# Kernel optimization log

Hardware: AMD Instinct MI355X
Metric: run time of the kernel (lower is better)

Reference implementation:

```python
import jax, jax.numpy as jnp
import numpy as np

FP8_MAX = 448.0  # torch.finfo(float8_e4m3fn).max
BLK = 128
EPS = 1e-12

def fp8_round(x):
    # saturated cast to float8_e4m3fn and back (emulates to_fp8_saturated)
    y = jnp.clip(x, -FP8_MAX, FP8_MAX)
    return y.astype(jnp.float8_e4m3fn).astype(jnp.float32)

def per_tile_quant_dequant(x):
    # activation: 1x128 tiles along the feature dim
    S, D = x.shape
    t = x.reshape(S, D // BLK, BLK)
    amax = jnp.max(jnp.abs(t), axis=-1, keepdims=True)
    scale = jnp.maximum(amax, EPS) / FP8_MAX
    q = fp8_round(t / scale)
    return (q * scale).reshape(S, D)

def per_block_quant_dequant_weight(w):
    # weight: 128x128 blocks, w is [ne, dout, din]
    ne, do, di = w.shape
    blk = w.reshape(ne, do // BLK, BLK, di // BLK, BLK)
    amax = jnp.max(jnp.abs(blk), axis=(2, 4), keepdims=True)
    scale = jnp.maximum(amax, EPS) / FP8_MAX
    q = fp8_round(blk / scale)
    return (q * scale).reshape(ne, do, di)

def setup_inputs() -> dict:
    key = jax.random.key(0)
    k1, k2 = jax.random.split(key)
    NE, DOUT, DIN, SEQ = 8, 1024, 2048, 16384
    x = jax.random.normal(k1, (SEQ, DIN), dtype=jnp.float32)
    w = jax.random.normal(k2, (NE * DOUT, DIN), dtype=jnp.float32) * 0.02
    tokens_per_expert = jnp.full((NE,), SEQ // NE, dtype=jnp.int32)
    return {"input": x, "tokens_per_expert": tokens_per_expert, "weight": w}

def reference(input, tokens_per_expert, weight):
    NE = tokens_per_expert.shape[0]
    S, DIN = input.shape
    DOUT = weight.shape[0] // NE
    w = weight.reshape(NE, DOUT, DIN)
    w_dq = per_block_quant_dequant_weight(w)   # fp8 per-block weight, dequantized
    x_dq = per_tile_quant_dequant(input)       # fp8 per-tile activation, dequantized
    # grouped varlen GEMM; tokens are split equally across experts here
    T = S // NE
    xe = x_dq.reshape(NE, T, DIN)
    out = jnp.einsum('etd,eod->eto', xe, w_dq)  # [ne, T, dout]
    return out.reshape(S, DOUT)
```

## Files before the change

kernel.cpp:

```cpp
#include <hip/hip_runtime.h>
#include <hip/hip_bf16.h>
#include <hip/hip_fp8.h>

#define SEQ   16384
#define DIN_  2048
#define DOUT_ 1024
#define NE_   8
#define TPE   (SEQ / NE_)
#define NG    (DIN_ / 128)

typedef float f32x4 __attribute__((ext_vector_type(4)));
typedef int   i32x4 __attribute__((ext_vector_type(4)));
typedef int   i32x8 __attribute__((ext_vector_type(8)));

#define GLD(gp, lp) __builtin_amdgcn_global_load_lds( \
    (const __attribute__((address_space(1))) unsigned int*)(gp), \
    (__attribute__((address_space(3))) unsigned int*)(lp), 16, 0, 0)

__device__ __forceinline__ unsigned char fp8_byte(float v, float scale) {
    float r = v / scale;
    r = fminf(fmaxf(r, -448.0f), 448.0f);
    __hip_fp8_e4m3 q(r);
    return (unsigned char)q.__x;
}

__global__ __launch_bounds__(256) void quant_x_kernel(const float* __restrict__ X,
                                                      unsigned char* __restrict__ Xq,
                                                      float* __restrict__ sxT) {
    const int row  = blockIdx.x;
    const int t    = threadIdx.x;
    const int lane = t & 63;
    const int wave = t >> 6;
    const int tile = wave * 4 + (lane >> 4);
    const int sub  = lane & 15;

    const float* p = X + (size_t)row * DIN_ + tile * 128 + sub * 8;
    float4 v0 = *(const float4*)p;
    float4 v1 = *(const float4*)(p + 4);

    float m = fmaxf(fmaxf(fmaxf(fabsf(v0.x), fabsf(v0.y)), fmaxf(fabsf(v0.z), fabsf(v0.w))),
                    fmaxf(fmaxf(fabsf(v1.x), fabsf(v1.y)), fmaxf(fabsf(v1.z), fabsf(v1.w))));
    #pragma unroll
    for (int off = 1; off < 16; off <<= 1)
        m = fmaxf(m, __shfl_xor(m, off, 64));

    const float scale = fmaxf(m, 1e-12f) / 448.0f;
    if (sub == 0) sxT[(size_t)tile * SEQ + row] = scale;

    unsigned lo = (unsigned)fp8_byte(v0.x, scale)
                | ((unsigned)fp8_byte(v0.y, scale) << 8)
                | ((unsigned)fp8_byte(v0.z, scale) << 16)
                | ((unsigned)fp8_byte(v0.w, scale) << 24);
    unsigned hi = (unsigned)fp8_byte(v1.x, scale)
                | ((unsigned)fp8_byte(v1.y, scale) << 8)
                | ((unsigned)fp8_byte(v1.z, scale) << 16)
                | ((unsigned)fp8_byte(v1.w, scale) << 24);
    uint2 u; u.x = lo; u.y = hi;
    *(uint2*)(Xq + (size_t)row * DIN_ + tile * 128 + sub * 8) = u;
}

__global__ __launch_bounds__(256) void quant_w_kernel(const float* __restrict__ W,
                                                      unsigned char* __restrict__ Wq,
                                                      float* __restrict__ sw) {
    const int rb = blockIdx.x >> 4;
    const int cb = blockIdx.x & 15;
    const int t  = threadIdx.x;

    const float* base = W + (size_t)(rb * 128) * DIN_ + cb * 128;
    const int r0 = t >> 5;
    const int c0 = (t & 31) * 4;

    float4 v[16];
    float m = 0.0f;
    #pragma unroll
    for (int i = 0; i < 16; ++i) {
        v[i] = *(const float4*)(base + (size_t)(i * 8 + r0) * DIN_ + c0);
        m = fmaxf(m, fmaxf(fmaxf(fabsf(v[i].x), fabsf(v[i].y)),
                           fmaxf(fabsf(v[i].z), fabsf(v[i].w))));
    }
    #pragma unroll
    for (int off = 1; off < 64; off <<= 1)
        m = fmaxf(m, __shfl_xor(m, off, 64));
    __shared__ float smx[4];
    if ((t & 63) == 0) smx[t >> 6] = m;
    __syncthreads();
    const float amax  = fmaxf(fmaxf(smx[0], smx[1]), fmaxf(smx[2], smx[3]));
    const float scale = fmaxf(amax, 1e-12f) / 448.0f;
    if (t == 0) sw[rb * 16 + cb] = scale;

    unsigned char* obase = Wq + (size_t)(rb * 128) * DIN_ + cb * 128;
    #pragma unroll
    for (int i = 0; i < 16; ++i) {
        unsigned u = (unsigned)fp8_byte(v[i].x, scale)
                   | ((unsigned)fp8_byte(v[i].y, scale) << 8)
                   | ((unsigned)fp8_byte(v[i].z, scale) << 16)
                   | ((unsigned)fp8_byte(v[i].w, scale) << 24);
        *(unsigned int*)(obase + (size_t)(i * 8 + r0) * DIN_ + c0) = u;
    }
}

__global__ __launch_bounds__(512, 2) void gemm_kernel(const unsigned char* __restrict__ Xq,
                                                      const unsigned char* __restrict__ Wq,
                                                      const float* __restrict__ sxT,
                                                      const float* __restrict__ sw,
                                                      float* __restrict__ out) {
    __shared__ unsigned char lds[147456];

    const int bid  = blockIdx.x;
    const int wgid = (bid & 7) * 32 + (bid >> 3);
    const int e    = wgid >> 5;
    const int tile = wgid & 31;
    const int brow = tile >> 2;
    const int bcol = tile & 3;

    const int t    = threadIdx.x;
    const int lane = t & 63;
    const int wave = t >> 6;
    const int wm   = wave >> 2;
    const int wn   = wave & 3;

    const int row0 = e * TPE + brow * 256;
    const unsigned char* Xt = Xq + (size_t)row0 * DIN_;
    const unsigned char* Wt = Wq + (size_t)(e * DOUT_ + bcol * 256) * DIN_;
    const float* swp = sw + (size_t)(e * 8 + bcol * 2 + (wn >> 1)) * 16;

    auto stage_group = [&](int g) {
        if (g >= NG) return;
        const unsigned abase = (unsigned)(g & 1) * 32768u;
        #pragma unroll
        for (int i = 0; i < 4; ++i) {
            const unsigned p = (unsigned)i * 8192u + (unsigned)t * 16u;
            const unsigned q = p ^ (((p >> 7) & 7u) << 4);
            GLD(Xt + (size_t)(q >> 7) * DIN_ + g * 128 + (q & 127u), &lds[abase + p]);
        }
        #pragma unroll
        for (int i = 0; i < 4; ++i) {
            const unsigned p = (unsigned)i * 8192u + (unsigned)t * 16u;
            const unsigned q = p ^ (((p >> 7) & 7u) << 4);
            GLD(Wt + (size_t)(q >> 7) * DIN_ + g * 128 + (q & 127u), &lds[65536u + abase + p]);
        }
    };

    auto ld_frag = [&](unsigned base, unsigned r) -> i32x8 {
        const unsigned kc  = (unsigned)(lane >> 4);
        const unsigned msk = (r & 7u) << 4;
        const unsigned p0  = (r * 128u + kc * 32u) ^ msk;
        const unsigned p1  = (r * 128u + kc * 32u + 16u) ^ msk;
        i32x4 lo = *(const i32x4*)&lds[base + p0];
        i32x4 hi = *(const i32x4*)&lds[base + p1];
        return __builtin_shufflevector(lo, hi, 0, 1, 2, 3, 4, 5, 6, 7);
    };
    auto ld_sx = [&](int m, int g) -> f32x4 {
        const unsigned r = (unsigned)(wm * 128 + m * 16 + ((lane >> 4) << 2));
        return *(const f32x4*)&lds[131072u + (unsigned)g * 1024u + r * 4u];
    };

    f32x4 acc[8][4] = {};
    const f32x4 zero = {0.f, 0.f, 0.f, 0.f};

    #pragma unroll
    for (int i = 0; i < 2; ++i) {
        const unsigned p = (unsigned)i * 8192u + (unsigned)t * 16u;
        GLD((const unsigned char*)sxT + ((size_t)(p >> 10) * SEQ + row0) * 4 + (p & 1023u),
            &lds[131072u + p]);
    }
    stage_group(0);
    stage_group(1);
    asm volatile("s_waitcnt vmcnt(8)" ::: "memory");
    __builtin_amdgcn_s_barrier();

    for (int g = 0; g < NG; ++g) {
        const unsigned abase = (unsigned)(g & 1) * 32768u;
        const unsigned bbase = 65536u + abase;
        const float swg = __uint_as_float(
            __builtin_amdgcn_readfirstlane(__float_as_uint(swp[g])));

        i32x8 bfr[4];
        #pragma unroll
        for (int n = 0; n < 4; ++n)
            bfr[n] = ld_frag(bbase, (unsigned)(wn * 64 + n * 16 + (lane & 15)));

        {
            i32x8 afr[4]; f32x4 sxv[4];
            #pragma unroll
            for (int m = 0; m < 4; ++m) {
                afr[m] = ld_frag(abase, (unsigned)(wm * 128 + m * 16 + (lane & 15)));
                sxv[m] = ld_sx(m, g);
            }
            asm volatile("s_waitcnt lgkmcnt(0)" ::: "memory");
            __builtin_amdgcn_sched_barrier(0);
            __builtin_amdgcn_s_setprio(1);
            #pragma unroll
            for (int m = 0; m < 4; ++m) {
                const f32x4 sf = sxv[m] * swg;
                #pragma unroll
                for (int n = 0; n < 4; ++n) {
                    f32x4 pn = __builtin_amdgcn_mfma_scale_f32_16x16x128_f8f6f4(
                        afr[m], bfr[n], zero, 0, 0, 0, 0x7f7f7f7f, 0, 0x7f7f7f7f);
                    acc[m][n] += pn * sf;
                }
            }
            __builtin_amdgcn_s_setprio(0);
        }

        {
            i32x8 afr[4]; f32x4 sxv[4];
            #pragma unroll
            for (int m = 0; m < 4; ++m) {
                afr[m] = ld_frag(abase, (unsigned)(wm * 128 + (m + 4) * 16 + (lane & 15)));
                sxv[m] = ld_sx(m + 4, g);
            }
            asm volatile("s_waitcnt lgkmcnt(0)" ::: "memory");
            __builtin_amdgcn_sched_barrier(0);
            __builtin_amdgcn_s_barrier();
            stage_group(g + 2);
            __builtin_amdgcn_s_setprio(1);
            #pragma unroll
            for (int m = 0; m < 4; ++m) {
                const f32x4 sf = sxv[m] * swg;
                #pragma unroll
                for (int n = 0; n < 4; ++n) {
                    f32x4 pn = __builtin_amdgcn_mfma_scale_f32_16x16x128_f8f6f4(
                        afr[m], bfr[n], zero, 0, 0, 0, 0x7f7f7f7f, 0, 0x7f7f7f7f);
                    acc[m + 4][n] += pn * sf;
                }
            }
            __builtin_amdgcn_s_setprio(0);
        }

        if (g < NG - 1) {
            if (g <= NG - 3)
                asm volatile("s_waitcnt vmcnt(8)" ::: "memory");
            else
                asm volatile("s_waitcnt vmcnt(0)" ::: "memory");
            __builtin_amdgcn_s_barrier();
        }
    }

    const int orow0 = e * TPE + brow * 256 + wm * 128;
    const int ocol0 = bcol * 256 + wn * 64;
    const int rl = (lane >> 4) * 4;
    const int cl = lane & 15;
    #pragma unroll
    for (int m = 0; m < 8; ++m)
        #pragma unroll
        for (int n = 0; n < 4; ++n)
            #pragma unroll
            for (int j = 0; j < 4; ++j) {
                const int r = orow0 + m * 16 + rl + j;
                const int c = ocol0 + n * 16 + cl;
                out[(size_t)r * DOUT_ + c] = acc[m][n][j];
            }
}

extern "C" void kernel_launch(void* const* d_in, const int* in_sizes, int n_in,
                              void* d_out, int out_size, void* d_ws, size_t ws_size,
                              hipStream_t stream) {
    const float* x = (const float*)d_in[0];
    const float* w = (const float*)d_in[2];
    float* out = (float*)d_out;

    unsigned char* xq = (unsigned char*)d_ws;
    unsigned char* wq = xq + (size_t)SEQ * DIN_;
    float* sxT = (float*)(wq + (size_t)NE_ * DOUT_ * DIN_);
    float* sw  = sxT + (size_t)NG * SEQ;

    quant_x_kernel<<<SEQ, 256, 0, stream>>>(x, xq, sxT);
    quant_w_kernel<<<(NE_ * DOUT_ / 128) * (DIN_ / 128), 256, 0, stream>>>(w, wq, sw);
    gemm_kernel<<<NE_ * (TPE / 256) * (DOUT_ / 256), 512, 0, stream>>>(xq, wq, sxT, sw, out);
}
```

Baseline: 140.8 us.

## Restructure GEMM loop schedule, stage weight scales in LDS, batch quant_x rows

The GEMM main loop is reordered. Next-group fragment reads for B, the first half of A and the scales are issued right after the barrier that follows staging. MFMAs are interleaved in pairs, so each scaled accumulate overlaps the next MFMA. Per-block weight scales are preloaded once into LDS instead of read from global each iteration. Separately, quant_x processes 4 rows per block, and both quant kernels multiply by a reciprocal instead of dividing. The reciprocal can change fp8 rounding slightly at boundary values.

```diff
diff --git a/kernel.cpp b/kernel.cpp
--- a/kernel.cpp
+++ b/kernel.cpp
@@ -17,8 +17,8 @@
     (const __attribute__((address_space(1))) unsigned int*)(gp), \
     (__attribute__((address_space(3))) unsigned int*)(lp), 16, 0, 0)
 
-__device__ __forceinline__ unsigned char fp8_byte(float v, float scale) {
-    float r = v / scale;
+__device__ __forceinline__ unsigned char fp8_byte_m(float v, float sinv) {
+    float r = v * sinv;
     r = fminf(fmaxf(r, -448.0f), 448.0f);
     __hip_fp8_e4m3 q(r);
     return (unsigned char)q.__x;
@@ -27,36 +27,48 @@
 __global__ __launch_bounds__(256) void quant_x_kernel(const float* __restrict__ X,
                                                       unsigned char* __restrict__ Xq,
                                                       float* __restrict__ sxT) {
-    const int row  = blockIdx.x;
     const int t    = threadIdx.x;
     const int lane = t & 63;
     const int wave = t >> 6;
     const int tile = wave * 4 + (lane >> 4);
     const int sub  = lane & 15;
-
-    const float* p = X + (size_t)row * DIN_ + tile * 128 + sub * 8;
-    float4 v0 = *(const float4*)p;
-    float4 v1 = *(const float4*)(p + 4);
-
-    float m = fmaxf(fmaxf(fmaxf(fabsf(v0.x), fabsf(v0.y)), fmaxf(fabsf(v0.z), fabsf(v0.w))),
-                    fmaxf(fmaxf(fabsf(v1.x), fabsf(v1.y)), fmaxf(fabsf(v1.z), fabsf(v1.w))));
-    #pragma unroll
-    for (int off = 1; off < 16; off <<= 1)
-        m = fmaxf(m, __shfl_xor(m, off, 64));
-
-    const float scale = fmaxf(m, 1e-12f) / 448.0f;
-    if (sub == 0) sxT[(size_t)tile * SEQ + row] = scale;
-
-    unsigned lo = (unsigned)fp8_byte(v0.x, scale)
-                | ((unsigned)fp8_byte(v0.y, scale) << 8)
-                | ((unsigned)fp8_byte(v0.z, scale) << 16)
-                | ((unsigned)fp8_byte(v0.w, scale) << 24);
-    unsigned hi = (unsigned)fp8_byte(v1.x, scale)
-                | ((unsigned)fp8_byte(v1.y, scale) << 8)
-                | ((unsigned)fp8_byte(v1.z, scale) << 16)
-                | ((unsigned)fp8_byte(v1.w, scale) << 24);
-    uint2 u; u.x = lo; u.y = hi;
-    *(uint2*)(Xq + (size_t)row * DIN_ + tile * 128 + sub * 8) = u;
+    const size_t off = (size_t)tile * 128 + sub * 8;
+
+    const int row0 = blockIdx.x * 4;
+    float4 v0[4], v1[4];
+    float mx[4];
+    #pragma unroll
+    for (int r = 0; r < 4; ++r) {
+        const float* p = X + (size_t)(row0 + r) * DIN_ + off;
+        v0[r] = *(const float4*)p;
+        v1[r] = *(const float4*)(p + 4);
+        mx[r] = fmaxf(fmaxf(fmaxf(fabsf(v0[r].x), fabsf(v0[r].y)),
+                            fmaxf(fabsf(v0[r].z), fabsf(v0[r].w))),
+                      fmaxf(fmaxf(fabsf(v1[r].x), fabsf(v1[r].y)),
+                            fmaxf(fabsf(v1[r].z), fabsf(v1[r].w))));
+    }
+    #pragma unroll
+    for (int o = 1; o < 16; o <<= 1) {
+        #pragma unroll
+        for (int r = 0; r < 4; ++r)
+            mx[r] = fmaxf(mx[r], __shfl_xor(mx[r], o, 64));
+    }
+    #pragma unroll
+    for (int r = 0; r < 4; ++r) {
+        const float s    = fmaxf(mx[r], 1e-12f) / 448.0f;
+        const float sinv = 1.0f / s;
+        if (sub == 0) sxT[(size_t)tile * SEQ + row0 + r] = s;
+        unsigned lo = (unsigned)fp8_byte_m(v0[r].x, sinv)
+                    | ((unsigned)fp8_byte_m(v0[r].y, sinv) << 8)
+                    | ((unsigned)fp8_byte_m(v0[r].z, sinv) << 16)
+                    | ((unsigned)fp8_byte_m(v0[r].w, sinv) << 24);
+        unsigned hi = (unsigned)fp8_byte_m(v1[r].x, sinv)
+                    | ((unsigned)fp8_byte_m(v1[r].y, sinv) << 8)
+                    | ((unsigned)fp8_byte_m(v1[r].z, sinv) << 16)
+                    | ((unsigned)fp8_byte_m(v1[r].w, sinv) << 24);
+        uint2 u; u.x = lo; u.y = hi;
+        *(uint2*)(Xq + (size_t)(row0 + r) * DIN_ + off) = u;
+    }
 }
 
 __global__ __launch_bounds__(256) void quant_w_kernel(const float* __restrict__ W,
@@ -84,17 +96,18 @@
     __shared__ float smx[4];
     if ((t & 63) == 0) smx[t >> 6] = m;
     __syncthreads();
-    const float amax  = fmaxf(fmaxf(smx[0], smx[1]), fmaxf(smx[2], smx[3]));
-    const float scale = fmaxf(amax, 1e-12f) / 448.0f;
-    if (t == 0) sw[rb * 16 + cb] = scale;
+    const float amax = fmaxf(fmaxf(smx[0], smx[1]), fmaxf(smx[2], smx[3]));
+    const float s    = fmaxf(amax, 1e-12f) / 448.0f;
+    const float sinv = 1.0f / s;
+    if (t == 0) sw[rb * 16 + cb] = s;
 
     unsigned char* obase = Wq + (size_t)(rb * 128) * DIN_ + cb * 128;
     #pragma unroll
     for (int i = 0; i < 16; ++i) {
-        unsigned u = (unsigned)fp8_byte(v[i].x, scale)
-                   | ((unsigned)fp8_byte(v[i].y, scale) << 8)
-                   | ((unsigned)fp8_byte(v[i].z, scale) << 16)
-                   | ((unsigned)fp8_byte(v[i].w, scale) << 24);
+        unsigned u = (unsigned)fp8_byte_m(v[i].x, sinv)
+                   | ((unsigned)fp8_byte_m(v[i].y, sinv) << 8)
+                   | ((unsigned)fp8_byte_m(v[i].z, sinv) << 16)
+                   | ((unsigned)fp8_byte_m(v[i].w, sinv) << 24);
         *(unsigned int*)(obase + (size_t)(i * 8 + r0) * DIN_ + c0) = u;
     }
 }
@@ -102,9 +115,9 @@
 __global__ __launch_bounds__(512, 2) void gemm_kernel(const unsigned char* __restrict__ Xq,
                                                       const unsigned char* __restrict__ Wq,
                                                       const float* __restrict__ sxT,
-                                                      const float* __restrict__ sw,
+                                                      const float* __restrict__ swg_,
                                                       float* __restrict__ out) {
-    __shared__ unsigned char lds[147456];
+    __shared__ __align__(16) unsigned char lds[147584];
 
     const int bid  = blockIdx.x;
     const int wgid = (bid & 7) * 32 + (bid >> 3);
@@ -118,45 +131,71 @@
     const int wave = t >> 6;
     const int wm   = wave >> 2;
     const int wn   = wave & 3;
+    const int fl   = lane & 15;
+    const unsigned kc  = (unsigned)(lane >> 4);
+    const unsigned sxr = (unsigned)((lane >> 4) * 4);
 
     const int row0 = e * TPE + brow * 256;
     const unsigned char* Xt = Xq + (size_t)row0 * DIN_;
     const unsigned char* Wt = Wq + (size_t)(e * DOUT_ + bcol * 256) * DIN_;
-    const float* swp = sw + (size_t)(e * 8 + bcol * 2 + (wn >> 1)) * 16;
-
-    auto stage_group = [&](int g) {
-        if (g >= NG) return;
-        const unsigned abase = (unsigned)(g & 1) * 32768u;
+
+    auto stage = [&](int j) {
+        if (j >= NG) return;
+        const unsigned ab = (unsigned)(j & 1) * 32768u;
         #pragma unroll
         for (int i = 0; i < 4; ++i) {
             const unsigned p = (unsigned)i * 8192u + (unsigned)t * 16u;
             const unsigned q = p ^ (((p >> 7) & 7u) << 4);
-            GLD(Xt + (size_t)(q >> 7) * DIN_ + g * 128 + (q & 127u), &lds[abase + p]);
+            GLD(Xt + (size_t)(q >> 7) * DIN_ + j * 128 + (q & 127u), &lds[ab + p]);
         }
         #pragma unroll
         for (int i = 0; i < 4; ++i) {
             const unsigned p = (unsigned)i * 8192u + (unsigned)t * 16u;
             const unsigned q = p ^ (((p >> 7) & 7u) << 4);
-            GLD(Wt + (size_t)(q >> 7) * DIN_ + g * 128 + (q & 127u), &lds[65536u + abase + p]);
+            GLD(Wt + (size_t)(q >> 7) * DIN_ + j * 128 + (q & 127u),
+                &lds[65536u + ab + p]);
         }
     };
 
-    auto ld_frag = [&](unsigned base, unsigned r) -> i32x8 {
-        const unsigned kc  = (unsigned)(lane >> 4);
-        const unsigned msk = (r & 7u) << 4;
-        const unsigned p0  = (r * 128u + kc * 32u) ^ msk;
-        const unsigned p1  = (r * 128u + kc * 32u + 16u) ^ msk;
-        i32x4 lo = *(const i32x4*)&lds[base + p0];
-        i32x4 hi = *(const i32x4*)&lds[base + p1];
+    auto ldf8 = [&](unsigned base, unsigned row) -> i32x8 {
+        const unsigned p0 = row * 128u + kc * 32u;
+        const unsigned s  = ((p0 >> 7) & 7u) << 4;
+        i32x4 lo = *(const i32x4*)&lds[base + (p0 ^ s)];
+        i32x4 hi = *(const i32x4*)&lds[base + ((p0 + 16u) ^ s)];
         return __builtin_shufflevector(lo, hi, 0, 1, 2, 3, 4, 5, 6, 7);
     };
-    auto ld_sx = [&](int m, int g) -> f32x4 {
-        const unsigned r = (unsigned)(wm * 128 + m * 16 + ((lane >> 4) << 2));
-        return *(const f32x4*)&lds[131072u + (unsigned)g * 1024u + r * 4u];
-    };
-
+
+    i32x8 bfr[4], aA[4], aB[4];
+    f32x4 sxv03[4], sxv47[4];
+    float swg;
     f32x4 acc[8][4] = {};
     const f32x4 zero = {0.f, 0.f, 0.f, 0.f};
+
+    #define AB_(buf) ((unsigned)(buf) * 32768u)
+    #define BB_(buf) (65536u + (unsigned)(buf) * 32768u)
+    #define MFS(a, b) __builtin_amdgcn_mfma_scale_f32_16x16x128_f8f6f4( \
+        a, b, zero, 0, 0, 0, 0x7f7f7f7f, 0, 0x7f7f7f7f)
+    #define TOP_READS(buf, g) \
+      { _Pragma("unroll") for (int n_ = 0; n_ < 4; ++n_) \
+            bfr[n_] = ldf8(BB_(buf), (unsigned)(wn * 64 + n_ * 16 + fl)); \
+        _Pragma("unroll") for (int m_ = 0; m_ < 4; ++m_) \
+            aA[m_] = ldf8(AB_(buf), (unsigned)(wm * 128 + m_ * 16 + fl)); \
+        _Pragma("unroll") for (int m_ = 0; m_ < 4; ++m_) \
+            sxv03[m_] = *(const f32x4*)&lds[131072u + (unsigned)(g) * 1024u \
+                + (unsigned)(wm * 128 + m_ * 16) * 4u + sxr * 4u]; \
+        swg = *(const float*)&lds[147456u + (unsigned)(((wn >> 1) << 4) + (g)) * 4u]; }
+    #define PHASE_MFMA(mo, afr, sxv) \
+      { f32x4 pnA[4], pnB[4]; \
+        const f32x4 sf0 = sxv[0] * swg, sf1 = sxv[1] * swg; \
+        const f32x4 sf2 = sxv[2] * swg, sf3 = sxv[3] * swg; \
+        _Pragma("unroll") for (int n_ = 0; n_ < 4; ++n_) pnA[n_] = MFS(afr[0], bfr[n_]); \
+        _Pragma("unroll") for (int n_ = 0; n_ < 4; ++n_) pnB[n_] = MFS(afr[1], bfr[n_]); \
+        _Pragma("unroll") for (int n_ = 0; n_ < 4; ++n_) acc[(mo)+0][n_] += pnA[n_] * sf0; \
+        _Pragma("unroll") for (int n_ = 0; n_ < 4; ++n_) pnA[n_] = MFS(afr[2], bfr[n_]); \
+        _Pragma("unroll") for (int n_ = 0; n_ < 4; ++n_) acc[(mo)+1][n_] += pnB[n_] * sf1; \
+        _Pragma("unroll") for (int n_ = 0; n_ < 4; ++n_) pnB[n_] = MFS(afr[3], bfr[n_]); \
+        _Pragma("unroll") for (int n_ = 0; n_ < 4; ++n_) acc[(mo)+2][n_] += pnA[n_] * sf2; \
+        _Pragma("unroll") for (int n_ = 0; n_ < 4; ++n_) acc[(mo)+3][n_] += pnB[n_] * sf3; }
 
     #pragma unroll
     for (int i = 0; i < 2; ++i) {
@@ -164,76 +203,44 @@
         GLD((const unsigned char*)sxT + ((size_t)(p >> 10) * SEQ + row0) * 4 + (p & 1023u),
             &lds[131072u + p]);
     }
-    stage_group(0);
-    stage_group(1);
+    float swv = 0.0f;
+    if (t < 32) swv = swg_[(size_t)(e * 8 + bcol * 2 + (t >> 4)) * 16 + (t & 15)];
+    stage(0); stage(1);
     asm volatile("s_waitcnt vmcnt(8)" ::: "memory");
+    if (t < 32) *(float*)&lds[147456u + (unsigned)t * 4u] = swv;
+    asm volatile("s_waitcnt lgkmcnt(0)" ::: "memory");
     __builtin_amdgcn_s_barrier();
+    TOP_READS(0, 0)
 
     for (int g = 0; g < NG; ++g) {
-        const unsigned abase = (unsigned)(g & 1) * 32768u;
-        const unsigned bbase = 65536u + abase;
-        const float swg = __uint_as_float(
-            __builtin_amdgcn_readfirstlane(__float_as_uint(swp[g])));
-
-        i32x8 bfr[4];
-        #pragma unroll
-        for (int n = 0; n < 4; ++n)
-            bfr[n] = ld_frag(bbase, (unsigned)(wn * 64 + n * 16 + (lane & 15)));
-
-        {
-            i32x8 afr[4]; f32x4 sxv[4];
-            #pragma unroll
-            for (int m = 0; m < 4; ++m) {
-                afr[m] = ld_frag(abase, (unsigned)(wm * 128 + m * 16 + (lane & 15)));
-                sxv[m] = ld_sx(m, g);
-            }
-            asm volatile("s_waitcnt lgkmcnt(0)" ::: "memory");
-            __builtin_amdgcn_sched_barrier(0);
-            __builtin_amdgcn_s_setprio(1);
-            #pragma unroll
-            for (int m = 0; m < 4; ++m) {
-                const f32x4 sf = sxv[m] * swg;
-                #pragma unroll
-                for (int n = 0; n < 4; ++n) {
-                    f32x4 pn = __builtin_amdgcn_mfma_scale_f32_16x16x128_f8f6f4(
-                        afr[m], bfr[n], zero, 0, 0, 0, 0x7f7f7f7f, 0, 0x7f7f7f7f);
-                    acc[m][n] += pn * sf;
-                }
-            }
-            __builtin_amdgcn_s_setprio(0);
-        }
-
-        {
-            i32x8 afr[4]; f32x4 sxv[4];
-            #pragma unroll
-            for (int m = 0; m < 4; ++m) {
-                afr[m] = ld_frag(abase, (unsigned)(wm * 128 + (m + 4) * 16 + (lane & 15)));
-                sxv[m] = ld_sx(m + 4, g);
-            }
-            asm volatile("s_waitcnt lgkmcnt(0)" ::: "memory");
-            __builtin_amdgcn_sched_barrier(0);
+        const int buf = g & 1;
+
+        asm volatile("s_waitcnt lgkmcnt(0)" ::: "memory");
+        __builtin_amdgcn_sched_barrier(0);
+        __builtin_amdgcn_s_setprio(1);
+        PHASE_MFMA(0, aA, sxv03)
+        __builtin_amdgcn_s_setprio(0);
+
+        #pragma unroll
+        for (int m_ = 0; m_ < 4; ++m_)
+            aB[m_] = ldf8(AB_(buf), (unsigned)(wm * 128 + (m_ + 4) * 16 + fl));
+        #pragma unroll
+        for (int m_ = 0; m_ < 4; ++m_)
+            sxv47[m_] = *(const f32x4*)&lds[131072u + (unsigned)g * 1024u
+                + (unsigned)(wm * 128 + (m_ + 4) * 16) * 4u + sxr * 4u];
+        asm volatile("s_waitcnt lgkmcnt(0)" ::: "memory");
+        __builtin_amdgcn_sched_barrier(0);
+        __builtin_amdgcn_s_setprio(1);
+        PHASE_MFMA(4, aB, sxv47)
+        __builtin_amdgcn_s_setprio(0);
+
+        if (g < NG - 1) {
             __builtin_amdgcn_s_barrier();
-            stage_group(g + 2);
-            __builtin_amdgcn_s_setprio(1);
-            #pragma unroll
-            for (int m = 0; m < 4; ++m) {
-                const f32x4 sf = sxv[m] * swg;
-                #pragma unroll
-                for (int n = 0; n < 4; ++n) {
-                    f32x4 pn = __builtin_amdgcn_mfma_scale_f32_16x16x128_f8f6f4(
-                        afr[m], bfr[n], zero, 0, 0, 0, 0x7f7f7f7f, 0, 0x7f7f7f7f);
-                    acc[m + 4][n] += pn * sf;
-                }
-            }
-            __builtin_amdgcn_s_setprio(0);
-        }
-
-        if (g < NG - 1) {
-            if (g <= NG - 3)
-                asm volatile("s_waitcnt vmcnt(8)" ::: "memory");
-            else
-                asm volatile("s_waitcnt vmcnt(0)" ::: "memory");
+            stage(g + 2);
+            if (g < NG - 2) asm volatile("s_waitcnt vmcnt(8)" ::: "memory");
+            else            asm volatile("s_waitcnt vmcnt(0)" ::: "memory");
             __builtin_amdgcn_s_barrier();
+            TOP_READS(buf ^ 1, g + 1)
         }
     }
 
@@ -265,7 +272,7 @@
     float* sxT = (float*)(wq + (size_t)NE_ * DOUT_ * DIN_);
     float* sw  = sxT + (size_t)NG * SEQ;
 
-    quant_x_kernel<<<SEQ, 256, 0, stream>>>(x, xq, sxT);
+    quant_x_kernel<<<SEQ / 4, 256, 0, stream>>>(x, xq, sxT);
     quant_w_kernel<<<(NE_ * DOUT_ / 128) * (DIN_ / 128), 256, 0, stream>>>(w, wq, sw);
     gemm_kernel<<<NE_ * (TPE / 256) * (DOUT_ / 256), 512, 0, stream>>>(xq, wq, sxT, sw, out);
 }
```

Measured after the change: 160.2 us. 1.14x slower.
